# Kernel optimization log

Hardware: AMD Instinct MI355X
Metric: run time of the kernel (lower is better)

The kernel has to match this reference:

```python
import jax, jax.numpy as jnp
import numpy as np
import math

L, Bt, IN, H = 512, 128, 512, 60


def setup_inputs() -> dict:
    key = jax.random.key(0)
    k1, k2, k3 = jax.random.split(key, 3)
    inp = jax.random.normal(k1, (L, Bt, IN), dtype=jnp.float32)
    W = jax.random.normal(k2, (H, IN), dtype=jnp.float32) / np.sqrt(IN)
    b = jnp.zeros((H,), dtype=jnp.float32)
    alphabet = jax.random.uniform(k3, (H, 3), dtype=jnp.float32, minval=-math.pi, maxval=math.pi)
    bond_lengths = jnp.array([132.868, 145.801, 152.326], dtype=jnp.float32)
    bond_angles = jnp.array([2.028, 2.124, 1.941], dtype=jnp.float32)
    return {"inp": inp, "W": W, "b": b, "alphabet": alphabet,
            "bond_lengths": bond_lengths, "bond_angles": bond_angles}


def reference(inp, W, b, alphabet, bond_lengths, bond_angles):
    Lr, Bb = inp.shape[0], inp.shape[1]
    # mixture over alphabet of torsion angles
    x = jax.nn.softmax(inp @ W.T + b, axis=2)                 # (L, B, H)
    phi = jnp.arctan2(x @ jnp.sin(alphabet), x @ jnp.cos(alphabet))  # (L, B, 3)
    # per residue i the loop consumes phi[i].T -> bond index is fastest axis
    phi_f = phi.transpose(0, 2, 1).reshape(Lr * 3, Bb)        # (3L, B)
    r = jnp.tile(bond_lengths, Lr)[:, None]                   # (3L, 1)
    th = jnp.tile(bond_angles, Lr)[:, None]                   # (3L, 1)
    # SRF coordinates of every new atom
    c_tilde = jnp.stack([
        (r * jnp.cos(th)) * jnp.ones_like(phi_f),
        r * jnp.cos(phi_f) * jnp.sin(th),
        r * jnp.sin(phi_f) * jnp.sin(th),
    ], axis=-1)                                               # (3L, B, 3)

    e = jnp.eye(3, dtype=inp.dtype)
    carry0 = (jnp.broadcast_to(e[0], (Bb, 3)),
              jnp.broadcast_to(e[1], (Bb, 3)),
              jnp.broadcast_to(e[2], (Bb, 3)))

    def step(carry, ct):
        A, Bp, C = carry                                      # each (B, 3)
        BC = C - Bp
        bc = BC / jnp.linalg.norm(BC, axis=1, keepdims=True)
        AB = Bp - A
        Nv = jnp.cross(AB, bc)
        n = Nv / jnp.linalg.norm(Nv, axis=1, keepdims=True)
        # D = C + R @ c_tilde, R columns = [bc, n x bc, n]
        D = C + bc * ct[:, 0:1] + jnp.cross(n, bc) * ct[:, 1:2] + n * ct[:, 2:3]
        return (Bp, C, D), D

    _, coords = jax.lax.scan(step, carry0, c_tilde)           # (3L, B, 3)
    return coords
```

## Files before the change

### kernel.cpp

```cpp
#include <hip/hip_runtime.h>
#include <math.h>

#define LSEQ  512
#define BT    128
#define INF   512
#define HH    60
#define NSTEP 1536
#define CHUNK 24

#define MTILE 128

typedef __attribute__((ext_vector_type(8))) short bf16x8;
typedef __attribute__((ext_vector_type(4))) float floatx4;

__device__ __forceinline__ unsigned short bf16_rn(float x) {
  unsigned u = __float_as_uint(x);
  return (unsigned short)((u + 0x7FFFu + ((u >> 16) & 1u)) >> 16);
}
__device__ __forceinline__ void split2(float x, unsigned short& h, unsigned short& l) {
  h = bf16_rn(x);
  float hf = __uint_as_float(((unsigned)h) << 16);
  l = bf16_rn(x - hf);
}

__global__ __launch_bounds__(256) void k_wconv(
    const float* __restrict__ W, unsigned short* __restrict__ Wh,
    unsigned short* __restrict__ Wl) {
  const int idx = blockIdx.x * 256 + threadIdx.x;
  const int h = idx >> 9, k = idx & 511;
  float x = (h < HH) ? W[h * INF + k] : 0.f;
  unsigned short hb, lb; split2(x, hb, lb);
  Wh[idx] = hb; Wl[idx] = lb;
}

__global__ __launch_bounds__(256, 2) void k_phi(
    const float* __restrict__ inp, const unsigned short* __restrict__ Wh,
    const unsigned short* __restrict__ Wl, const float* __restrict__ bias,
    const float* __restrict__ alphabet, float* __restrict__ phi_out) {
  __shared__ float sS[HH * 3], sC[HH * 3], sBias[64];

  const int tid  = threadIdx.x;
  const int lane = tid & 63;
  const int wid  = tid >> 6;
  const int c    = lane & 15;
  const int quad = lane >> 4;
  const int row0 = blockIdx.x * MTILE;

  if (tid < HH * 3) { float a = alphabet[tid]; sS[tid] = __sinf(a); sC[tid] = __cosf(a); }
  if (tid >= 192 && tid < 256) { int n = tid - 192; sBias[n] = (n < HH) ? bias[n] : 0.f; }

  floatx4 acc[2][4];
#pragma unroll
  for (int mt = 0; mt < 2; ++mt)
#pragma unroll
    for (int nt = 0; nt < 4; ++nt) acc[mt][nt] = (floatx4){0.f, 0.f, 0.f, 0.f};

  const float* a0p = inp + (size_t)(row0 + wid * 32 + c)      * INF + quad * 8;
  const float* a1p = inp + (size_t)(row0 + wid * 32 + 16 + c) * INF + quad * 8;
  const unsigned short* whp = Wh + (size_t)c * INF + quad * 8;
  const unsigned short* wlp = Wl + (size_t)c * INF + quad * 8;

#pragma unroll 2
  for (int ks = 0; ks < INF / 32; ++ks) {
    const int kg = ks * 32;
    float4 a00 = *(const float4*)(a0p + kg);
    float4 a01 = *(const float4*)(a0p + kg + 4);
    float4 a10 = *(const float4*)(a1p + kg);
    float4 a11 = *(const float4*)(a1p + kg + 4);
    bf16x8 Bh[4], Bl[4];
#pragma unroll
    for (int nt = 0; nt < 4; ++nt) {
      Bh[nt] = *(const bf16x8*)(whp + (size_t)(nt * 16) * INF + kg);
      Bl[nt] = *(const bf16x8*)(wlp + (size_t)(nt * 16) * INF + kg);
    }
    bf16x8 Ah[2], Al[2];
    {
      float av[2][8] = {{a00.x,a00.y,a00.z,a00.w,a01.x,a01.y,a01.z,a01.w},
                        {a10.x,a10.y,a10.z,a10.w,a11.x,a11.y,a11.z,a11.w}};
#pragma unroll
      for (int mt = 0; mt < 2; ++mt)
#pragma unroll
        for (int j = 0; j < 8; ++j) {
          unsigned short hb, lb; split2(av[mt][j], hb, lb);
          Ah[mt][j] = (short)hb; Al[mt][j] = (short)lb;
        }
    }
#pragma unroll
    for (int mt = 0; mt < 2; ++mt)
#pragma unroll
      for (int nt = 0; nt < 4; ++nt) {
        acc[mt][nt] = __builtin_amdgcn_mfma_f32_16x16x32_bf16(Ah[mt], Bh[nt], acc[mt][nt], 0, 0, 0);
        acc[mt][nt] = __builtin_amdgcn_mfma_f32_16x16x32_bf16(Ah[mt], Bl[nt], acc[mt][nt], 0, 0, 0);
        acc[mt][nt] = __builtin_amdgcn_mfma_f32_16x16x32_bf16(Al[mt], Bh[nt], acc[mt][nt], 0, 0, 0);
      }
  }

  __syncthreads();

#pragma unroll
  for (int mt = 0; mt < 2; ++mt) {
#pragma unroll
    for (int reg = 0; reg < 4; ++reg) {
      float lg[4];  bool val[4];
#pragma unroll
      for (int nt = 0; nt < 4; ++nt) {
        const int n = nt * 16 + c;
        val[nt] = (n < HH);
        lg[nt] = acc[mt][nt][reg] + sBias[n];
      }
      float m = -1e30f;
#pragma unroll
      for (int nt = 0; nt < 4; ++nt) if (val[nt]) m = fmaxf(m, lg[nt]);
#pragma unroll
      for (int d = 1; d < 16; d <<= 1) m = fmaxf(m, __shfl_xor(m, d, 64));

      float s0=0.f,c0=0.f,s1=0.f,c1=0.f,s2=0.f,c2=0.f;
#pragma unroll
      for (int nt = 0; nt < 4; ++nt) {
        const int n = nt * 16 + c;
        float e = val[nt] ? __expf(lg[nt] - m) : 0.f;
        s0 = fmaf(e, sS[n*3+0], s0);  c0 = fmaf(e, sC[n*3+0], c0);
        s1 = fmaf(e, sS[n*3+1], s1);  c1 = fmaf(e, sC[n*3+1], c1);
        s2 = fmaf(e, sS[n*3+2], s2);  c2 = fmaf(e, sC[n*3+2], c2);
      }
#pragma unroll
      for (int d = 1; d < 16; d <<= 1) {
        s0 += __shfl_xor(s0, d, 64);  c0 += __shfl_xor(c0, d, 64);
        s1 += __shfl_xor(s1, d, 64);  c1 += __shfl_xor(c1, d, 64);
        s2 += __shfl_xor(s2, d, 64);  c2 += __shfl_xor(c2, d, 64);
      }
      if (c == 0) {
        const int row = row0 + wid * 32 + mt * 16 + quad * 4 + reg;
        const int l  = row >> 7;
        const int bb = row & 127;
        float* pp = phi_out + (size_t)bb * NSTEP + 3 * l;
        pp[0] = atan2f(s0, c0);
        pp[1] = atan2f(s1, c1);
        pp[2] = atan2f(s2, c2);
      }
    }
  }
}

struct Xf { float r[9]; float p[3]; };

__device__ __forceinline__ Xf compose(const Xf& A, const Xf& B) {
  Xf o;
#pragma unroll
  for (int i = 0; i < 3; ++i) {
#pragma unroll
    for (int j = 0; j < 3; ++j) {
      o.r[i*3+j] = fmaf(A.r[i*3+0], B.r[0+j],
                   fmaf(A.r[i*3+1], B.r[3+j],
                        A.r[i*3+2] * B.r[6+j]));
    }
    o.p[i] = fmaf(A.r[i*3+0], B.p[0],
             fmaf(A.r[i*3+1], B.p[1],
             fmaf(A.r[i*3+2], B.p[2], A.p[i])));
  }
  return o;
}

__device__ __forceinline__ Xf make_T(float phi, float st, float ct, float r) {
  float sp = __sinf(phi), cp = __cosf(phi);
  Xf T;
  T.r[0] = ct;      T.r[1] = -st;     T.r[2] = 0.f;
  T.r[3] = cp * st; T.r[4] = ct * cp; T.r[5] = -sp;
  T.r[6] = sp * st; T.r[7] = ct * sp; T.r[8] = cp;
  T.p[0] = r * ct;  T.p[1] = r * T.r[3]; T.p[2] = r * T.r[6];
  return T;
}

__device__ __forceinline__ void set_identity(Xf& X) {
  X.r[0]=1.f; X.r[1]=0.f; X.r[2]=0.f;
  X.r[3]=0.f; X.r[4]=1.f; X.r[5]=0.f;
  X.r[6]=0.f; X.r[7]=0.f; X.r[8]=1.f;
  X.p[0]=0.f; X.p[1]=0.f; X.p[2]=0.f;
}

__global__ __launch_bounds__(64) void k_scan(
    const float* __restrict__ phi, const float* __restrict__ bl,
    const float* __restrict__ ba, float* __restrict__ out) {
  const int b = blockIdx.x;
  const int t = threadIdx.x;

  float st[3], ct[3], rr[3];
#pragma unroll
  for (int j = 0; j < 3; ++j) {
    float a = ba[j];
    st[j] = __sinf(a); ct[j] = __cosf(a); rr[j] = bl[j];
  }

  float f[CHUNK];
  const float4* ph4 = (const float4*)(phi + (size_t)b * NSTEP + t * CHUNK);
#pragma unroll
  for (int q = 0; q < CHUNK/4; ++q) {
    float4 v = ph4[q];
    f[4*q+0] = v.x; f[4*q+1] = v.y; f[4*q+2] = v.z; f[4*q+3] = v.w;
  }

  Xf Q = make_T(f[0], st[0], ct[0], rr[0]);
#pragma unroll
  for (int s = 1; s < CHUNK; ++s)
    Q = compose(Q, make_T(f[s], st[s%3], ct[s%3], rr[s%3]));

#pragma unroll
  for (int d = 1; d < 64; d <<= 1) {
    Xf O;
#pragma unroll
    for (int q = 0; q < 9; ++q) O.r[q] = __shfl_up(Q.r[q], d, 64);
#pragma unroll
    for (int q = 0; q < 3; ++q) O.p[q] = __shfl_up(Q.p[q], d, 64);
    if (t < d) set_identity(O);
    Q = compose(O, Q);
  }

  Xf E;
#pragma unroll
  for (int q = 0; q < 9; ++q) E.r[q] = __shfl_up(Q.r[q], 1, 64);
#pragma unroll
  for (int q = 0; q < 3; ++q) E.p[q] = __shfl_up(Q.p[q], 1, 64);
  if (t == 0) set_identity(E);

  Xf S0;
  S0.r[0] = 0.f;                  S0.r[1] = 0.816496580927726f;   S0.r[2] = 0.5773502691896258f;
  S0.r[3] = -0.7071067811865475f; S0.r[4] = -0.4082482904638631f; S0.r[5] = 0.5773502691896258f;
  S0.r[6] = 0.7071067811865475f;  S0.r[7] = -0.4082482904638631f; S0.r[8] = 0.5773502691896258f;
  S0.p[0] = 0.f; S0.p[1] = 0.f; S0.p[2] = 1.f;

  Xf cur = compose(S0, E);

  float* op = out + (size_t)(t * CHUNK) * (BT * 3) + b * 3;
#pragma unroll
  for (int s = 0; s < CHUNK; ++s) {
    cur = compose(cur, make_T(f[s], st[s%3], ct[s%3], rr[s%3]));
    op[(size_t)s * (BT*3) + 0] = cur.p[0];
    op[(size_t)s * (BT*3) + 1] = cur.p[1];
    op[(size_t)s * (BT*3) + 2] = cur.p[2];
  }
}

extern "C" void kernel_launch(void* const* d_in, const int* in_sizes, int n_in,
                              void* d_out, int out_size, void* d_ws, size_t ws_size,
                              hipStream_t stream) {
  const float* inp      = (const float*)d_in[0];
  const float* W        = (const float*)d_in[1];
  const float* bias     = (const float*)d_in[2];
  const float* alphabet = (const float*)d_in[3];
  const float* bl       = (const float*)d_in[4];
  const float* ba       = (const float*)d_in[5];
  float* out = (float*)d_out;

  float* phi = (float*)d_ws;
  unsigned short* Wh = (unsigned short*)((char*)d_ws + 786432);
  unsigned short* Wl = Wh + 64 * INF;

  k_wconv<<<dim3(128), dim3(256), 0, stream>>>(W, Wh, Wl);
  k_phi<<<dim3((LSEQ*BT)/MTILE), dim3(256), 0, stream>>>(inp, Wh, Wl, bias, alphabet, phi);
  k_scan<<<dim3(BT), dim3(64), 0, stream>>>(phi, bl, ba, out);
}
```

Measured before the change: 234.0 us.

## Stage split bf16 weights in LDS per K-half and prefetch A tiles

The GEMM kernel now copies the high and low bf16 weight tiles for half of K into padded shared memory, one half at a time. All four waves then read B fragments from LDS instead of each issuing its own global loads. The A-operand float loads are software-prefetched one k-step ahead to hide global latency. This adds about 67 KB of LDS per block and an extra barrier, which may lower occupancy below the two blocks per CU requested by the launch bounds.

```diff
diff --git a/kernel.cpp b/kernel.cpp
--- a/kernel.cpp
+++ b/kernel.cpp
@@ -9,6 +9,7 @@
 #define CHUNK 24
 
 #define MTILE 128
+#define BROW  264
 
 typedef __attribute__((ext_vector_type(8))) short bf16x8;
 typedef __attribute__((ext_vector_type(4))) float floatx4;
@@ -37,6 +38,8 @@
     const float* __restrict__ inp, const unsigned short* __restrict__ Wh,
     const unsigned short* __restrict__ Wl, const float* __restrict__ bias,
     const float* __restrict__ alphabet, float* __restrict__ phi_out) {
+  __shared__ unsigned short BhL[64 * BROW];
+  __shared__ unsigned short BlL[64 * BROW];
   __shared__ float sS[HH * 3], sC[HH * 3], sBias[64];
 
   const int tid  = threadIdx.x;
@@ -55,47 +58,67 @@
 #pragma unroll
     for (int nt = 0; nt < 4; ++nt) acc[mt][nt] = (floatx4){0.f, 0.f, 0.f, 0.f};
 
-  const float* a0p = inp + (size_t)(row0 + wid * 32 + c)      * INF + quad * 8;
-  const float* a1p = inp + (size_t)(row0 + wid * 32 + 16 + c) * INF + quad * 8;
-  const unsigned short* whp = Wh + (size_t)c * INF + quad * 8;
-  const unsigned short* wlp = Wl + (size_t)c * INF + quad * 8;
-
-#pragma unroll 2
-  for (int ks = 0; ks < INF / 32; ++ks) {
-    const int kg = ks * 32;
-    float4 a00 = *(const float4*)(a0p + kg);
-    float4 a01 = *(const float4*)(a0p + kg + 4);
-    float4 a10 = *(const float4*)(a1p + kg);
-    float4 a11 = *(const float4*)(a1p + kg + 4);
-    bf16x8 Bh[4], Bl[4];
-#pragma unroll
-    for (int nt = 0; nt < 4; ++nt) {
-      Bh[nt] = *(const bf16x8*)(whp + (size_t)(nt * 16) * INF + kg);
-      Bl[nt] = *(const bf16x8*)(wlp + (size_t)(nt * 16) * INF + kg);
-    }
-    bf16x8 Ah[2], Al[2];
-    {
-      float av[2][8] = {{a00.x,a00.y,a00.z,a00.w,a01.x,a01.y,a01.z,a01.w},
-                        {a10.x,a10.y,a10.z,a10.w,a11.x,a11.y,a11.z,a11.w}};
+  const float* ap0 = inp + (size_t)(row0 + wid * 32 + c)      * INF + quad * 8;
+  const float* ap1 = ap0 + 16 * INF;
+
+  for (int half = 0; half < 2; ++half) {
+    const int kbase = half * 256;
+    if (half) __syncthreads();
+#pragma unroll
+    for (int i = 0; i < 8; ++i) {
+      const int chunk = i * 256 + tid;
+      const int r = chunk >> 5;
+      const int j = (chunk & 31) * 8;
+      *(uint4*)&BhL[r * BROW + j] = *(const uint4*)(Wh + (size_t)r * INF + kbase + j);
+      *(uint4*)&BlL[r * BROW + j] = *(const uint4*)(Wl + (size_t)r * INF + kbase + j);
+    }
+    __syncthreads();
+
+    float4 pa0, pa1, pa2, pa3;
+    pa0 = *(const float4*)(ap0 + kbase);
+    pa1 = *(const float4*)(ap0 + kbase + 4);
+    pa2 = *(const float4*)(ap1 + kbase);
+    pa3 = *(const float4*)(ap1 + kbase + 4);
+
+#pragma unroll
+    for (int ks = 0; ks < 8; ++ks) {
+      const int kl = ks * 32;
+      float4 a00 = pa0, a01 = pa1, a10 = pa2, a11 = pa3;
+      if (ks + 1 < 8) {
+        pa0 = *(const float4*)(ap0 + kbase + kl + 32);
+        pa1 = *(const float4*)(ap0 + kbase + kl + 36);
+        pa2 = *(const float4*)(ap1 + kbase + kl + 32);
+        pa3 = *(const float4*)(ap1 + kbase + kl + 36);
+      }
+      bf16x8 Bh[4], Bl[4];
+#pragma unroll
+      for (int nt = 0; nt < 4; ++nt) {
+        const int boff = (nt * 16 + c) * BROW + kl + quad * 8;
+        Bh[nt] = *(const bf16x8*)&BhL[boff];
+        Bl[nt] = *(const bf16x8*)&BlL[boff];
+      }
+      bf16x8 Ah[2], Al[2];
+      {
+        float av[2][8] = {{a00.x,a00.y,a00.z,a00.w,a01.x,a01.y,a01.z,a01.w},
+                          {a10.x,a10.y,a10.z,a10.w,a11.x,a11.y,a11.z,a11.w}};
+#pragma unroll
+        for (int mt = 0; mt < 2; ++mt)
+#pragma unroll
+          for (int j = 0; j < 8; ++j) {
+            unsigned short hb, lb; split2(av[mt][j], hb, lb);
+            Ah[mt][j] = (short)hb; Al[mt][j] = (short)lb;
+          }
+      }
 #pragma unroll
       for (int mt = 0; mt < 2; ++mt)
 #pragma unroll
-        for (int j = 0; j < 8; ++j) {
-          unsigned short hb, lb; split2(av[mt][j], hb, lb);
-          Ah[mt][j] = (short)hb; Al[mt][j] = (short)lb;
+        for (int nt = 0; nt < 4; ++nt) {
+          acc[mt][nt] = __builtin_amdgcn_mfma_f32_16x16x32_bf16(Ah[mt], Bh[nt], acc[mt][nt], 0, 0, 0);
+          acc[mt][nt] = __builtin_amdgcn_mfma_f32_16x16x32_bf16(Ah[mt], Bl[nt], acc[mt][nt], 0, 0, 0);
+          acc[mt][nt] = __builtin_amdgcn_mfma_f32_16x16x32_bf16(Al[mt], Bh[nt], acc[mt][nt], 0, 0, 0);
         }
     }
-#pragma unroll
-    for (int mt = 0; mt < 2; ++mt)
-#pragma unroll
-      for (int nt = 0; nt < 4; ++nt) {
-        acc[mt][nt] = __builtin_amdgcn_mfma_f32_16x16x32_bf16(Ah[mt], Bh[nt], acc[mt][nt], 0, 0, 0);
-        acc[mt][nt] = __builtin_amdgcn_mfma_f32_16x16x32_bf16(Ah[mt], Bl[nt], acc[mt][nt], 0, 0, 0);
-        acc[mt][nt] = __builtin_amdgcn_mfma_f32_16x16x32_bf16(Al[mt], Bh[nt], acc[mt][nt], 0, 0, 0);
-      }
-  }
-
-  __syncthreads();
+  }
 
 #pragma unroll
   for (int mt = 0; mt < 2; ++mt) {
```

Measured after the change: 221.8 us. 1.06x faster.
